# Kernel tuning notes

Hardware: AMD Instinct MI355X
Metric: run time of the kernel (lower is better)

## Reference

```python
import jax, jax.numpy as jnp
import numpy as np

D_MODEL = 1024
N_HEADS = 16
HEAD_DIM = D_MODEL // N_HEADS


def setup_inputs() -> dict:
    key = jax.random.key(0)
    ks = jax.random.split(key, 6)
    B, T, S = 4, 1024, 2048
    scale = 1.0 / np.sqrt(D_MODEL)
    return {
        "query": jax.random.normal(ks[0], (B, T, D_MODEL), jnp.float32),
        "key_value": jax.random.normal(ks[1], (B, S, D_MODEL), jnp.float32),
        "wq": jax.random.normal(ks[2], (D_MODEL, D_MODEL), jnp.float32) * scale,
        "wk": jax.random.normal(ks[3], (D_MODEL, D_MODEL), jnp.float32) * scale,
        "wv": jax.random.normal(ks[4], (D_MODEL, D_MODEL), jnp.float32) * scale,
        "wo": jax.random.normal(ks[5], (D_MODEL, D_MODEL), jnp.float32) * scale,
    }


def reference(query, key_value, wq, wk, wv, wo):
    B, T, _ = query.shape
    S = key_value.shape[1]
    # projections (nn.Linear with weight W computes x @ W.T; here wq etc. are W)
    q = (query @ wq.T).reshape(B, T, N_HEADS, HEAD_DIM)
    k = (key_value @ wk.T).reshape(B, S, N_HEADS, HEAD_DIM)
    v = (key_value @ wv.T).reshape(B, S, N_HEADS, HEAD_DIM)
    scale = HEAD_DIM ** -0.5
    attn = jnp.einsum("bthd,bshd->bhts", q, k) * scale  # [B,H,T,S]
    attn = jax.nn.softmax(attn, axis=-1)
    out = jnp.einsum("bhts,bshd->bthd", attn, v).reshape(B, T, N_HEADS * HEAD_DIM)
    return out @ wo.T
```

## Files before the change

kernel.cpp:

```cpp
#include <hip/hip_runtime.h>
#include <cstdint>
#include <cstddef>

#define N_HEADS 16

typedef __attribute__((ext_vector_type(4))) float f32x4;
typedef __attribute__((ext_vector_type(8))) short bf16x8;

static __device__ inline ushort f2bf(float x) {
    uint32_t u = __float_as_uint(x);
    uint32_t r = (u + 0x7fffu + ((u >> 16) & 1u)) >> 16;
    return (ushort)r;
}
static __device__ inline float bf2f(ushort h) {
    return __uint_as_float(((uint32_t)h) << 16);
}
static __device__ inline uint32_t cvt_pk_bf16(float lo, float hi) {
    uint32_t r;
    asm("v_cvt_pk_bf16_f32 %0, %1, %2" : "=v"(r) : "v"(lo), "v"(hi));
    return r;
}
static __device__ inline float exp2_raw(float x) {
    float r;
    asm("v_exp_f32 %0, %1" : "=v"(r) : "v"(x));
    return r;
}

__global__ __launch_bounds__(256) void split_all(
    const float* __restrict__ query, const float* __restrict__ keyv,
    const float* __restrict__ wq, const float* __restrict__ wk,
    const float* __restrict__ wv, const float* __restrict__ wo,
    ushort* __restrict__ inq_h, ushort* __restrict__ inkv_h,
    ushort* __restrict__ wqh, ushort* __restrict__ wkh,
    ushort* __restrict__ wvh, ushort* __restrict__ woh,
    ushort* __restrict__ wol) {
    const float* x;
    ushort* hi;
    ushort* lo = nullptr;
    int n4;
    switch (blockIdx.y) {
        case 0: x = query; hi = inq_h;           n4 = 1048576; break;
        case 1: x = keyv;  hi = inkv_h;          n4 = 2097152; break;
        case 2: x = wq;    hi = wqh;             n4 = 262144;  break;
        case 3: x = wk;    hi = wkh;             n4 = 262144;  break;
        case 4: x = wv;    hi = wvh;             n4 = 262144;  break;
        default: x = wo;   hi = woh; lo = wol;   n4 = 262144;  break;
    }
    const int stride = gridDim.x * blockDim.x;
    const bool wlo = (lo != nullptr);
    for (int i = blockIdx.x * blockDim.x + threadIdx.x; i < n4; i += stride) {
        const float4 v = reinterpret_cast<const float4*>(x)[i];
        ushort4 h;
        h.x = f2bf(v.x); h.y = f2bf(v.y); h.z = f2bf(v.z); h.w = f2bf(v.w);
        reinterpret_cast<ushort4*>(hi)[i] = h;
        if (wlo) {
            ushort4 l;
            l.x = f2bf(v.x - bf2f(h.x)); l.y = f2bf(v.y - bf2f(h.y));
            l.z = f2bf(v.z - bf2f(h.z)); l.w = f2bf(v.w - bf2f(h.w));
            reinterpret_cast<ushort4*>(lo)[i] = l;
        }
    }
}

#define BM 128
#define BN 128
#define BK 32

#define GLD_LDS16(gp, lp)                                                  \
    __builtin_amdgcn_global_load_lds(                                      \
        (const __attribute__((address_space(1))) void*)(gp),               \
        (__attribute__((address_space(3))) void*)(lp), 16, 0, 0)

__global__ __launch_bounds__(256, 3) void qkv_proj(
    const ushort* __restrict__ Aq, const ushort* __restrict__ Akv,
    const ushort* __restrict__ Wqh, const ushort* __restrict__ Wkh,
    const ushort* __restrict__ Wvh, ushort* __restrict__ aq,
    ushort* __restrict__ ak, ushort* __restrict__ avt) {
    constexpr int K = 1024;
    constexpr float QSCALE = 0.18033688011112042f;
    __shared__ ushort sA[BM * BK];
    __shared__ ushort sB[BN * BK];

    const int bid = blockIdx.x;
    int seg, local, nrow;
    if (bid < 256)      { seg = 0; local = bid;       nrow = 32; }
    else if (bid < 768) { seg = 1; local = bid - 256; nrow = 64; }
    else                { seg = 2; local = bid - 768; nrow = 64; }
    local = (local & 7) * nrow + (local >> 3);
    const int n0 = (local & 7) * BN;
    const int m0 = (local >> 3) * BM;

    const ushort* A  = (seg == 0) ? Aq : Akv;
    const ushort* Wh = (seg == 0) ? Wqh : (seg == 1 ? Wkh : Wvh);

    const int tid = threadIdx.x;
    const int lane = tid & 63;
    const int w = tid >> 6;
    const int wm = (w >> 1) * 64;
    const int wn = (w & 1) * 64;

    int srow[2], skq[2];
#pragma unroll
    for (int c = 0; c < 2; ++c) {
        const int row = (w * 2 + c) * 16 + (lane >> 2);
        srow[c] = row;
        skq[c] = (((lane & 3) ^ ((row >> 1) & 3)) << 3);
    }

    f32x4 acc[4][4];
#pragma unroll
    for (int i = 0; i < 4; ++i)
#pragma unroll
        for (int j = 0; j < 4; ++j) acc[i][j] = (f32x4)0.0f;

    const int lr = lane & 15;
    const int kq = lane >> 4;

    for (int k0 = 0; k0 < K; k0 += BK) {
#pragma unroll
        for (int c = 0; c < 2; ++c) {
            const size_t ga = (size_t)(m0 + srow[c]) * K + k0 + skq[c];
            const size_t gb = (size_t)(n0 + srow[c]) * K + k0 + skq[c];
            const int loff = (w * 2 + c) * 512;
            GLD_LDS16(A + ga, &sA[loff]);
            GLD_LDS16(Wh + gb, &sB[loff]);
        }
        __syncthreads();

        bf16x8 afh[4], bfh[4];
#pragma unroll
        for (int f = 0; f < 4; ++f) {
            const int arow = wm + f * 16 + lr;
            afh[f] = *reinterpret_cast<const bf16x8*>(
                &sA[arow * 32 + ((kq ^ ((arow >> 1) & 3)) << 3)]);
            const int brow = wn + f * 16 + lr;
            bfh[f] = *reinterpret_cast<const bf16x8*>(
                &sB[brow * 32 + ((kq ^ ((brow >> 1) & 3)) << 3)]);
        }
#pragma unroll
        for (int i = 0; i < 4; ++i)
#pragma unroll
            for (int j = 0; j < 4; ++j)
                acc[i][j] = __builtin_amdgcn_mfma_f32_16x16x32_bf16(
                    afh[i], bfh[j], acc[i][j], 0, 0, 0);
        __syncthreads();
    }

    const int cr = (lane >> 4) << 2;
    const int cc = lane & 15;

    if (seg < 2) {
        const int log2X = (seg == 0) ? 10 : 11;
        const float scale = (seg == 0) ? QSCALE : 1.0f;
        ushort* out = (seg == 0) ? aq : ak;
        const int xm = (1 << log2X) - 1;
#pragma unroll
        for (int i = 0; i < 4; ++i)
#pragma unroll
            for (int j = 0; j < 4; ++j) {
                const int col = n0 + wn + j * 16 + cc;
                const int h = col >> 6, dd = col & 63;
#pragma unroll
                for (int r = 0; r < 4; ++r) {
                    const int mr = m0 + wm + i * 16 + cr + r;
                    const int bb = mr >> log2X;
                    const int x = mr & xm;
                    out[(((size_t)(bb * N_HEADS + h) << log2X) + x) * 64 +
                        (dd ^ ((x & 7) << 3))] = f2bf(acc[i][j][r] * scale);
                }
            }
    } else {
#pragma unroll
        for (int i = 0; i < 4; ++i)
#pragma unroll
            for (int j = 0; j < 4; ++j) {
                const int col = n0 + wn + j * 16 + cc;
                const int h = col >> 6, dd = col & 63;
                const int sb = m0 + wm + i * 16 + cr;
                const int bb = sb >> 11;
                const int sx = sb & 2047;
                ushort4 hv;
#pragma unroll
                for (int r = 0; r < 4; ++r)
                    ((ushort*)&hv)[r] = f2bf(acc[i][j][r]);
                const size_t pos =
                    ((size_t)(bb * N_HEADS + h) * 64 + dd) * 2048 +
                    (sx & ~63) + ((sx & 63) ^ ((dd & 7) << 3));
                *reinterpret_cast<ushort4*>(&avt[pos]) = hv;
            }
    }
}

#define OBM 64
__global__ __launch_bounds__(256, 2) void gemm_oproj(
    const ushort* __restrict__ Ahi, const ushort* __restrict__ Whi,
    const ushort* __restrict__ Wlo, float* __restrict__ Cf, int M, int N,
    int K) {
    __shared__ ushort sA[OBM * BK];
    __shared__ ushort sB[2][BN * BK];

    const int tid = threadIdx.x;
    const int lane = tid & 63;
    const int w = tid >> 6;
    const int m0 = blockIdx.y * OBM;
    const int n0 = blockIdx.x * BN;

    const int sarow = w * 16 + (lane >> 2);
    const int saq = (((lane & 3) ^ ((sarow >> 1) & 3)) << 3);
    int srow[2], skq[2];
#pragma unroll
    for (int c = 0; c < 2; ++c) {
        const int row = (w * 2 + c) * 16 + (lane >> 2);
        srow[c] = row;
        skq[c] = (((lane & 3) ^ ((row >> 1) & 3)) << 3);
    }

    f32x4 acc[8];
#pragma unroll
    for (int j = 0; j < 8; ++j) acc[j] = (f32x4)0.0f;

    const int lr = lane & 15;
    const int kq = lane >> 4;

    for (int k0 = 0; k0 < K; k0 += BK) {
        GLD_LDS16(Ahi + (size_t)(m0 + sarow) * K + k0 + saq, &sA[w * 512]);
#pragma unroll
        for (int c = 0; c < 2; ++c) {
            const size_t gb = (size_t)(n0 + srow[c]) * K + k0 + skq[c];
            const int loff = (w * 2 + c) * 512;
            GLD_LDS16(Whi + gb, &sB[0][loff]);
            GLD_LDS16(Wlo + gb, &sB[1][loff]);
        }
        __syncthreads();

        const int arow = w * 16 + lr;
        const bf16x8 afh = *reinterpret_cast<const bf16x8*>(
            &sA[arow * 32 + ((kq ^ ((arow >> 1) & 3)) << 3)]);
#pragma unroll
        for (int j = 0; j < 8; ++j) {
            const int brow = j * 16 + lr;
            const int boff = brow * 32 + ((kq ^ ((brow >> 1) & 3)) << 3);
            const bf16x8 bfh = *reinterpret_cast<const bf16x8*>(&sB[0][boff]);
            const bf16x8 bfl = *reinterpret_cast<const bf16x8*>(&sB[1][boff]);
            acc[j] = __builtin_amdgcn_mfma_f32_16x16x32_bf16(afh, bfh,
                                                             acc[j], 0, 0, 0);
            acc[j] = __builtin_amdgcn_mfma_f32_16x16x32_bf16(afh, bfl,
                                                             acc[j], 0, 0, 0);
        }
        __syncthreads();
    }

    const int cr = (lane >> 4) << 2;
    const int cc = lane & 15;
#pragma unroll
    for (int j = 0; j < 8; ++j) {
        float* cp = &Cf[(size_t)(m0 + w * 16 + cr) * N + n0 + j * 16 + cc];
#pragma unroll
        for (int r = 0; r < 4; ++r) cp[(size_t)r * N] = acc[j][r];
    }
}

__global__ __launch_bounds__(256, 4) void attn_mfma(
    const ushort* __restrict__ Qhi, const ushort* __restrict__ Khi,
    const ushort* __restrict__ Vhi, ushort* __restrict__ Ohi) {
    constexpr int T = 1024, S = 2048, NT = S / 64;
    __shared__ ushort sK[2][4096];
    __shared__ ushort sV[2][4096];
    __shared__ ushort sPb[4096];

    const int tid = threadIdx.x;
    const int lane = tid & 63;
    const int w = tid >> 6;
    const int id = blockIdx.x;
    const int wid = (id & 7) * 128 + (id >> 3);
    const int t0 = (wid & 15) * 64;
    const int bh = wid >> 4;
    const int lr = lane & 15;
    const int g = lane >> 4;
    const int swz = (lr & 7) << 3;

    const size_t qbase = ((size_t)bh * T + t0) * 64;
    const size_t kbase = (size_t)bh * S * 64;
    const size_t vbase = (size_t)bh * 64;

    int loff[2];
    const ushort* kp[2];
    const ushort* vp[2];
#pragma unroll
    for (int i = 0; i < 2; ++i) {
        loff[i] = i * 2048 + w * 512 + lane * 8;
        kp[i] = Khi + kbase + loff[i];
        vp[i] = Vhi + (vbase + (loff[i] >> 6)) * S + (loff[i] & 63);
    }

    int rdoff[4][2], pwoff[4], proff[2];
#pragma unroll
    for (int j = 0; j < 4; ++j) {
#pragma unroll
        for (int kk = 0; kk < 2; ++kk)
            rdoff[j][kk] = (j * 16 + lr) * 64 + ((kk * 32 + g * 8) ^ swz);
        pwoff[j] = lr * 64 + ((j * 16 + g * 4) ^ swz);
    }
#pragma unroll
    for (int kk = 0; kk < 2; ++kk)
        proff[kk] = lr * 64 + ((kk * 32 + g * 8) ^ swz);

#pragma unroll
    for (int i = 0; i < 2; ++i) GLD_LDS16(Qhi + qbase + loff[i], &sK[1][loff[i]]);
#pragma unroll
    for (int i = 0; i < 2; ++i) {
        GLD_LDS16(kp[i], &sK[0][loff[i]]);
        GLD_LDS16(vp[i], &sV[0][loff[i]]);
        kp[i] += 4096;
        vp[i] += 64;
    }
    __syncthreads();

    bf16x8 qf[2];
#pragma unroll
    for (int kk = 0; kk < 2; ++kk)
        qf[kk] = *reinterpret_cast<const bf16x8*>(
            &sK[1][(w * 16 + lr) * 64 + ((kk * 32 + g * 8) ^ swz)]);
    __syncthreads();

    ushort* sP = &sPb[w * 1024];

    f32x4 oacc[4];
#pragma unroll
    for (int jd = 0; jd < 4; ++jd) oacc[jd] = (f32x4)0.0f;
    const f32x4 zero4 = (f32x4)0.0f;
    float lpart = 0.0f;

    for (int t = 0; t < NT; ++t) {
        const int bi = t & 1;
        if (t + 1 < NT) {
#pragma unroll
            for (int i = 0; i < 2; ++i) {
                GLD_LDS16(kp[i], &sK[bi ^ 1][loff[i]]);
                GLD_LDS16(vp[i], &sV[bi ^ 1][loff[i]]);
                kp[i] += 4096;
                vp[i] += 64;
            }
        }

        f32x4 sacc[4];
        __builtin_amdgcn_s_setprio(1);
#pragma unroll
        for (int j = 0; j < 4; ++j) {
            const bf16x8 kh0 = *reinterpret_cast<const bf16x8*>(
                &sK[bi][rdoff[j][0]]);
            const bf16x8 kh1 = *reinterpret_cast<const bf16x8*>(
                &sK[bi][rdoff[j][1]]);
            sacc[j] = __builtin_amdgcn_mfma_f32_16x16x32_bf16(
                kh0, qf[0], zero4, 0, 0, 0);
            sacc[j] = __builtin_amdgcn_mfma_f32_16x16x32_bf16(
                kh1, qf[1], sacc[j], 0, 0, 0);
        }
        __builtin_amdgcn_s_setprio(0);

        uint32_t wpk[4][2];
#pragma unroll
        for (int j = 0; j < 4; ++j) {
            const float p0 = exp2_raw(sacc[j][0]);
            const float p1 = exp2_raw(sacc[j][1]);
            const float p2 = exp2_raw(sacc[j][2]);
            const float p3 = exp2_raw(sacc[j][3]);
            lpart += (p0 + p1) + (p2 + p3);
            wpk[j][0] = cvt_pk_bf16(p0, p1);
            wpk[j][1] = cvt_pk_bf16(p2, p3);
        }

#pragma unroll
        for (int j = 0; j < 4; ++j)
            *reinterpret_cast<uint2*>(&sP[pwoff[j]]) =
                make_uint2(wpk[j][0], wpk[j][1]);
        asm volatile("s_waitcnt lgkmcnt(0)" ::: "memory");
        __builtin_amdgcn_sched_barrier(0);

        bf16x8 pf[2];
#pragma unroll
        for (int kk = 0; kk < 2; ++kk)
            pf[kk] = *reinterpret_cast<const bf16x8*>(&sP[proff[kk]]);
        __builtin_amdgcn_s_setprio(1);
#pragma unroll
        for (int jd = 0; jd < 4; ++jd) {
#pragma unroll
            for (int kk = 0; kk < 2; ++kk) {
                const bf16x8 vh = *reinterpret_cast<const bf16x8*>(
                    &sV[bi][rdoff[jd][kk]]);
                oacc[jd] = __builtin_amdgcn_mfma_f32_16x16x32_bf16(
                    pf[kk], vh, oacc[jd], 0, 0, 0);
            }
        }
        __builtin_amdgcn_s_setprio(0);
        __syncthreads();
    }

    float l = lpart;
    l += __shfl_xor(l, 16);
    l += __shfl_xor(l, 32);

    const int b = bh >> 4, h = bh & 15;
    float linv[4];
#pragma unroll
    for (int r = 0; r < 4; ++r) linv[r] = 1.0f / __shfl(l, g * 4 + r);
#pragma unroll
    for (int r = 0; r < 4; ++r) {
        const int q = t0 + w * 16 + g * 4 + r;
        const size_t rowb = ((size_t)(b * T + q)) * 1024 + h * 64;
#pragma unroll
        for (int jd = 0; jd < 4; ++jd)
            Ohi[rowb + jd * 16 + lr] = f2bf(oacc[jd][r] * linv[r]);
    }
}

extern "C" void kernel_launch(void* const* d_in, const int* in_sizes, int n_in,
                              void* d_out, int out_size, void* d_ws, size_t ws_size,
                              hipStream_t stream) {
    const int B = 4, T = 1024, S = 2048, D = 1024;

    const float* query = (const float*)d_in[0];
    const float* keyv  = (const float*)d_in[1];
    const float* wq    = (const float*)d_in[2];
    const float* wk    = (const float*)d_in[3];
    const float* wv    = (const float*)d_in[4];
    const float* wo    = (const float*)d_in[5];
    float* out = (float*)d_out;

    const size_t nQ = (size_t)B * T * D;
    const size_t nK = (size_t)B * S * D;
    const size_t nW = (size_t)D * D;

    uint8_t* p = (uint8_t*)d_ws;
    ushort* inq_h = (ushort*)p;  p += nQ * 2;
    ushort* inkv_h = (ushort*)p; p += nK * 2;
    ushort* wqh = (ushort*)p;    p += nW * 2;
    ushort* wkh = (ushort*)p;    p += nW * 2;
    ushort* wvh = (ushort*)p;    p += nW * 2;
    ushort* woh = (ushort*)p;    p += nW * 2;
    ushort* wol = (ushort*)p;    p += nW * 2;
    ushort* aq_h = (ushort*)p;   p += nQ * 2;
    ushort* ak_h = (ushort*)p;   p += nK * 2;
    ushort* avt_h = (ushort*)p;  p += nK * 2;
    ushort* ao_h = (ushort*)p;   p += nQ * 2;

    const dim3 blk(256);

    split_all<<<dim3(512, 6), blk, 0, stream>>>(
        query, keyv, wq, wk, wv, wo, inq_h, inkv_h, wqh, wkh, wvh, woh, wol);

    qkv_proj<<<dim3(1280), blk, 0, stream>>>(inq_h, inkv_h, wqh, wkh, wvh,
                                             aq_h, ak_h, avt_h);

    attn_mfma<<<dim3((T / 64) * B * N_HEADS), blk, 0, stream>>>(
        aq_h, ak_h, avt_h, ao_h);

    gemm_oproj<<<dim3(D / BN, (B * T) / OBM), blk, 0, stream>>>(
        ao_h, woh, wol, out, B * T, D, D);
}
```

Baseline: 156.9 us.

## Fuse fp32-to-bf16 activation conversion into QKV projection loads

```diff
diff --git a/kernel.cpp b/kernel.cpp
--- a/kernel.cpp
+++ b/kernel.cpp
@@ -26,26 +26,22 @@
     return r;
 }
 
-__global__ __launch_bounds__(256) void split_all(
-    const float* __restrict__ query, const float* __restrict__ keyv,
+__global__ __launch_bounds__(256) void split_w(
     const float* __restrict__ wq, const float* __restrict__ wk,
     const float* __restrict__ wv, const float* __restrict__ wo,
-    ushort* __restrict__ inq_h, ushort* __restrict__ inkv_h,
     ushort* __restrict__ wqh, ushort* __restrict__ wkh,
     ushort* __restrict__ wvh, ushort* __restrict__ woh,
     ushort* __restrict__ wol) {
     const float* x;
     ushort* hi;
     ushort* lo = nullptr;
-    int n4;
     switch (blockIdx.y) {
-        case 0: x = query; hi = inq_h;           n4 = 1048576; break;
-        case 1: x = keyv;  hi = inkv_h;          n4 = 2097152; break;
-        case 2: x = wq;    hi = wqh;             n4 = 262144;  break;
-        case 3: x = wk;    hi = wkh;             n4 = 262144;  break;
-        case 4: x = wv;    hi = wvh;             n4 = 262144;  break;
-        default: x = wo;   hi = woh; lo = wol;   n4 = 262144;  break;
-    }
+        case 0: x = wq; hi = wqh; break;
+        case 1: x = wk; hi = wkh; break;
+        case 2: x = wv; hi = wvh; break;
+        default: x = wo; hi = woh; lo = wol; break;
+    }
+    const int n4 = 262144;
     const int stride = gridDim.x * blockDim.x;
     const bool wlo = (lo != nullptr);
     for (int i = blockIdx.x * blockDim.x + threadIdx.x; i < n4; i += stride) {
@@ -72,7 +68,7 @@
         (__attribute__((address_space(3))) void*)(lp), 16, 0, 0)
 
 __global__ __launch_bounds__(256, 3) void qkv_proj(
-    const ushort* __restrict__ Aq, const ushort* __restrict__ Akv,
+    const float* __restrict__ Aqf, const float* __restrict__ Akvf,
     const ushort* __restrict__ Wqh, const ushort* __restrict__ Wkh,
     const ushort* __restrict__ Wvh, ushort* __restrict__ aq,
     ushort* __restrict__ ak, ushort* __restrict__ avt) {
@@ -90,7 +86,7 @@
     const int n0 = (local & 7) * BN;
     const int m0 = (local >> 3) * BM;
 
-    const ushort* A  = (seg == 0) ? Aq : Akv;
+    const float* Af  = (seg == 0) ? Aqf : Akvf;
     const ushort* Wh = (seg == 0) ? Wqh : (seg == 1 ? Wkh : Wvh);
 
     const int tid = threadIdx.x;
@@ -119,11 +115,18 @@
     for (int k0 = 0; k0 < K; k0 += BK) {
 #pragma unroll
         for (int c = 0; c < 2; ++c) {
-            const size_t ga = (size_t)(m0 + srow[c]) * K + k0 + skq[c];
-            const size_t gb = (size_t)(n0 + srow[c]) * K + k0 + skq[c];
-            const int loff = (w * 2 + c) * 512;
-            GLD_LDS16(A + ga, &sA[loff]);
-            GLD_LDS16(Wh + gb, &sB[loff]);
+            const float* ap =
+                Af + (size_t)(m0 + srow[c]) * K + k0 + skq[c];
+            const float4 a0 = *reinterpret_cast<const float4*>(ap);
+            const float4 a1 = *reinterpret_cast<const float4*>(ap + 4);
+            uint4 pk;
+            pk.x = cvt_pk_bf16(a0.x, a0.y);
+            pk.y = cvt_pk_bf16(a0.z, a0.w);
+            pk.z = cvt_pk_bf16(a1.x, a1.y);
+            pk.w = cvt_pk_bf16(a1.z, a1.w);
+            *reinterpret_cast<uint4*>(&sA[(w * 2 + c) * 512 + lane * 8]) = pk;
+            GLD_LDS16(Wh + (size_t)(n0 + srow[c]) * K + k0 + skq[c],
+                      &sB[(w * 2 + c) * 512]);
         }
         __syncthreads();
 
@@ -432,8 +435,6 @@
     const size_t nW = (size_t)D * D;
 
     uint8_t* p = (uint8_t*)d_ws;
-    ushort* inq_h = (ushort*)p;  p += nQ * 2;
-    ushort* inkv_h = (ushort*)p; p += nK * 2;
     ushort* wqh = (ushort*)p;    p += nW * 2;
     ushort* wkh = (ushort*)p;    p += nW * 2;
     ushort* wvh = (ushort*)p;    p += nW * 2;
@@ -446,10 +447,10 @@
 
     const dim3 blk(256);
 
-    split_all<<<dim3(512, 6), blk, 0, stream>>>(
-        query, keyv, wq, wk, wv, wo, inq_h, inkv_h, wqh, wkh, wvh, woh, wol);
-
-    qkv_proj<<<dim3(1280), blk, 0, stream>>>(inq_h, inkv_h, wqh, wkh, wvh,
+    split_w<<<dim3(128, 4), blk, 0, stream>>>(wq, wk, wv, wo, wqh, wkh, wvh,
+                                              woh, wol);
+
+    qkv_proj<<<dim3(1280), blk, 0, stream>>>(query, keyv, wqh, wkh, wvh,
                                              aq_h, ak_h, avt_h);
 
     attn_mfma<<<dim3((T / 64) * B * N_HEADS), blk, 0, stream>>>(
```

After: 156.7 us (median of 2 runs). About the same (-0.1%).
